# Kernel tuning notes

Measured on AMD Instinct MI355X. Metric: run time of the kernel, lower is better.

## Reference

```python
import jax, jax.numpy as jnp
import numpy as np

N_NODES = 100000
N_EDGES = 1600000
IN_CH = 128
OUT_CH = 32
HID = 2 * OUT_CH


def setup_inputs() -> dict:
    key = jax.random.key(0)
    k1, k2, k3, k4 = jax.random.split(key, 4)
    x = jax.random.normal(k1, (N_NODES, IN_CH), dtype=jnp.float32)
    edge_index = jax.random.randint(k2, (2, N_EDGES), 0, N_NODES, dtype=jnp.int64)
    W1 = jax.random.normal(k3, (IN_CH, HID), dtype=jnp.float32) / np.sqrt(IN_CH)
    b1 = jnp.zeros((HID,), dtype=jnp.float32)
    W2 = jax.random.normal(k4, (HID, OUT_CH), dtype=jnp.float32) / np.sqrt(HID)
    b2 = jnp.zeros((OUT_CH,), dtype=jnp.float32)
    return {"x": x, "edge_index": edge_index, "W1": W1, "b1": b1, "W2": W2, "b2": b2}


def _gcn_norm(edge_index, n_nodes):
    # GCNConv default: add self-loops, symmetric deg^{-1/2} normalization.
    loop = jnp.arange(n_nodes, dtype=edge_index.dtype)
    src = jnp.concatenate([edge_index[0], loop])
    dst = jnp.concatenate([edge_index[1], loop])
    deg = jax.ops.segment_sum(jnp.ones_like(dst, dtype=jnp.float32), dst, num_segments=n_nodes)
    dinv = jnp.where(deg > 0, jax.lax.rsqrt(deg), 0.0)
    norm = dinv[src] * dinv[dst]  # [E + N]
    return src, dst, norm


def _gcn_conv(h, W, b, src, dst, norm, n_nodes):
    m = h @ W                      # transform first (small GEMM)
    msg = m[src] * norm[:, None]   # gather + scale per edge
    agg = jax.ops.segment_sum(msg, dst, num_segments=n_nodes)  # scatter-add
    return agg + b


def reference(x, edge_index, W1, b1, W2, b2):
    n = x.shape[0]
    src, dst, norm = _gcn_norm(edge_index, n)
    h = jax.nn.relu(_gcn_conv(x, W1, b1, src, dst, norm, n))
    return _gcn_conv(h, W2, b2, src, dst, norm, n)
```

## Files before the change

kernel.cpp:

```cpp
#include <hip/hip_runtime.h>

#define IN_CH 128
#define HID 64
#define OUT_CH 32
#define BUCKET_CAP 6144
#define NB_MAX 512

typedef _Float16 f16x8 __attribute__((ext_vector_type(8)));
typedef float f32x4 __attribute__((ext_vector_type(4)));

__device__ __forceinline__ unsigned short f32_to_bf16(float f) {
    union { float f; unsigned int u; } v; v.f = f;
    unsigned int u = v.u;
    u += 0x7FFFu + ((u >> 16) & 1u);
    return (unsigned short)(u >> 16);
}
__device__ __forceinline__ float bf16_to_f32(unsigned short h) {
    union { unsigned int u; float f; } v; v.u = ((unsigned int)h) << 16;
    return v.f;
}
__device__ __forceinline__ float bf16_lo(unsigned int u) {
    union { unsigned int u; float f; } v; v.u = u << 16; return v.f;
}
__device__ __forceinline__ float bf16_hi(unsigned int u) {
    union { unsigned int u; float f; } v; v.u = u & 0xFFFF0000u; return v.f;
}

__device__ __forceinline__ int load_idx(const void* e, long long i, int is64) {
    if (is64) return ((const int*)e)[2 * i];
    return ((const int*)e)[i];
}

__global__ __launch_bounds__(256) void binA_kernel(
    const void* __restrict__ edges, long long E,
    int* __restrict__ bucket_cur, unsigned int* __restrict__ entries, int nb) {
    __shared__ int hist[NB_MAX];
    __shared__ int cbase[NB_MAX];
    __shared__ int s_is64;
    const int tid = threadIdx.x;

    if (tid < 64) {
        int v = ((const int*)edges)[2 * tid + 1];
        unsigned long long nz = __ballot(v != 0);
        if (tid == 0) s_is64 = (nz == 0ull) ? 1 : 0;
    }
    for (int i = tid; i < nb; i += 256) hist[i] = 0;
    __syncthreads();
    const int is64 = s_is64;

    const long long per = (E + gridDim.x - 1) / gridDim.x;
    const long long lo = blockIdx.x * per;
    const long long hi = (lo + per < E) ? lo + per : E;

    for (long long i = lo + tid; i < hi; i += 256) {
        int dst = load_idx(edges, E + i, is64);
        atomicAdd(&hist[dst >> 8], 1);
    }
    __syncthreads();
    for (int i = tid; i < nb; i += 256) {
        int c = hist[i];
        int base = (c > 0) ? atomicAdd(&bucket_cur[i], c) : 0;
        cbase[i] = base;
        hist[i] = 0;
    }
    __syncthreads();
    for (long long i = lo + tid; i < hi; i += 256) {
        int src = load_idx(edges, i, is64);
        int dst = load_idx(edges, E + i, is64);
        int b = dst >> 8;
        int rel = cbase[b] + atomicAdd(&hist[b], 1);
        if (rel < BUCKET_CAP)
            entries[(long long)b * BUCKET_CAP + rel] = ((unsigned)src << 8) | (unsigned)(dst & 255);
    }
}

__global__ __launch_bounds__(256) void binB1_kernel(
    const unsigned int* __restrict__ entries, const int* __restrict__ bucket_cur,
    int* __restrict__ counts, int* __restrict__ row_off, float* __restrict__ dinv,
    int n) {
    __shared__ int hist[256];
    __shared__ int scan[256];
    const int b   = blockIdx.x;
    const int tid = threadIdx.x;
    const long long seg = (long long)b * BUCKET_CAP;
    int cnt = bucket_cur[b];
    if (cnt > BUCKET_CAP) cnt = BUCKET_CAP;

    hist[tid] = 0;
    __syncthreads();
    for (int i = tid; i < cnt; i += 256)
        atomicAdd(&hist[entries[seg + i] & 255], 1);
    __syncthreads();

    int v = hist[tid];
    scan[tid] = v;
    __syncthreads();
    for (int off = 1; off < 256; off <<= 1) {
        int t = (tid >= off) ? scan[tid - off] : 0;
        __syncthreads();
        scan[tid] += t;
        __syncthreads();
    }
    int ex = scan[tid] - v;
    int node = (b << 8) + tid;
    if (node < n) {
        counts[node]  = v;
        row_off[node] = (int)seg + ex;
        dinv[node]    = rsqrtf((float)v + 1.0f);
    }
}

__global__ __launch_bounds__(256) void binB2_kernel(
    const unsigned int* __restrict__ entries, const int* __restrict__ bucket_cur,
    const int* __restrict__ row_off, const float* __restrict__ dinv,
    int2* __restrict__ ew, int n) {
    __shared__ int cur[256];
    __shared__ float ldi[256];
    const int b   = blockIdx.x;
    const int tid = threadIdx.x;
    const long long seg = (long long)b * BUCKET_CAP;
    int cnt = bucket_cur[b];
    if (cnt > BUCKET_CAP) cnt = BUCKET_CAP;

    int node = (b << 8) + tid;
    cur[tid] = (node < n) ? row_off[node] - (int)seg : 0;
    ldi[tid] = (node < n) ? dinv[node] : 0.f;
    __syncthreads();

    for (int i = tid; i < cnt; i += 256) {
        unsigned e = entries[seg + i];
        int d = (int)(e & 255u);
        int s = (int)(e >> 8);
        int r = atomicAdd(&cur[d], 1);
        float w = dinv[s] * ldi[d];
        int2 o; o.x = s; o.y = __float_as_int(w);
        ew[seg + r] = o;
    }
}

__global__ __launch_bounds__(256) void gemm1_kernel(
    const float* __restrict__ x, const float* __restrict__ W1,
    unsigned short* __restrict__ m1bf, int n) {
    const int lane = threadIdx.x & 63;
    const int wid  = threadIdx.x >> 6;
    const int m    = lane & 15;
    const int g    = lane >> 4;
    const int Rw   = blockIdx.x * 64 + wid * 16;

    f16x8 wf[4][4];
#pragma unroll
    for (int t = 0; t < 4; ++t) {
        const float* wp = W1 + (t * 32 + g * 8) * HID + m;
#pragma unroll
        for (int c = 0; c < 4; ++c) {
#pragma unroll
            for (int j = 0; j < 8; ++j)
                wf[c][t][j] = (_Float16)wp[j * HID + c * 16];
        }
    }

    int rl = Rw + m;
    if (rl >= n) rl = n - 1;
    const float* xr = x + (long long)rl * IN_CH;

    f32x4 acc[4] = {};

#pragma unroll
    for (int t = 0; t < 4; ++t) {
        float4 xa = *(const float4*)(xr + t * 32 + g * 8);
        float4 xb = *(const float4*)(xr + t * 32 + g * 8 + 4);
        f16x8 af;
        af[0] = (_Float16)xa.x; af[1] = (_Float16)xa.y;
        af[2] = (_Float16)xa.z; af[3] = (_Float16)xa.w;
        af[4] = (_Float16)xb.x; af[5] = (_Float16)xb.y;
        af[6] = (_Float16)xb.z; af[7] = (_Float16)xb.w;
#pragma unroll
        for (int c = 0; c < 4; ++c)
            acc[c] = __builtin_amdgcn_mfma_f32_16x16x32_f16(af, wf[c][t], acc[c], 0, 0, 0);
    }

#pragma unroll
    for (int c = 0; c < 4; ++c) {
#pragma unroll
        for (int r = 0; r < 4; ++r) {
            int row = Rw + g * 4 + r;
            if (row < n)
                m1bf[(long long)row * HID + c * 16 + m] = f32_to_bf16(acc[c][r]);
        }
    }
}

#define PADH 132
__global__ __launch_bounds__(256) void gemm2_kernel(
    const unsigned short* __restrict__ hbf, const float* __restrict__ W2,
    unsigned short* __restrict__ m2bf, int n) {
    __shared__ __align__(16) float sW[HID * OUT_CH];
    __shared__ __align__(16) float sH[HID * PADH];
    const int tid = threadIdx.x;

    {
        const float4* Wv = (const float4*)W2;
        float4* sWv = (float4*)sW;
        for (int i = tid; i < HID * OUT_CH / 4; i += 256) sWv[i] = Wv[i];
    }

    const int R0 = blockIdx.x * 128;
    for (int i = tid; i < 128 * 8; i += 256) {
        int r = i >> 3;
        int q = i & 7;
        int row = R0 + r;
        uint4 v = make_uint4(0u, 0u, 0u, 0u);
        if (row < n)
            v = ((const uint4*)(hbf + (long long)row * HID))[q];
        int k0 = q * 8;
        sH[(k0 + 0) * PADH + r] = bf16_lo(v.x);
        sH[(k0 + 1) * PADH + r] = bf16_hi(v.x);
        sH[(k0 + 2) * PADH + r] = bf16_lo(v.y);
        sH[(k0 + 3) * PADH + r] = bf16_hi(v.y);
        sH[(k0 + 4) * PADH + r] = bf16_lo(v.z);
        sH[(k0 + 5) * PADH + r] = bf16_hi(v.z);
        sH[(k0 + 6) * PADH + r] = bf16_lo(v.w);
        sH[(k0 + 7) * PADH + r] = bf16_hi(v.w);
    }
    __syncthreads();

    const int tx = tid & 7;
    const int ty = tid >> 3;
    float acc[4][4] = {};
    const float* pH = sH + ty * 4;
    const float* pW = sW + tx * 4;
#pragma unroll 8
    for (int k = 0; k < HID; ++k) {
        float4 hv = *(const float4*)(pH + k * PADH);
        float4 wv = *(const float4*)(pW + k * OUT_CH);
        acc[0][0] += hv.x * wv.x; acc[0][1] += hv.x * wv.y;
        acc[0][2] += hv.x * wv.z; acc[0][3] += hv.x * wv.w;
        acc[1][0] += hv.y * wv.x; acc[1][1] += hv.y * wv.y;
        acc[1][2] += hv.y * wv.z; acc[1][3] += hv.y * wv.w;
        acc[2][0] += hv.z * wv.x; acc[2][1] += hv.z * wv.y;
        acc[2][2] += hv.z * wv.z; acc[2][3] += hv.z * wv.w;
        acc[3][0] += hv.w * wv.x; acc[3][1] += hv.w * wv.y;
        acc[3][2] += hv.w * wv.z; acc[3][3] += hv.w * wv.w;
    }

#pragma unroll
    for (int i = 0; i < 4; ++i) {
        int row = R0 + ty * 4 + i;
        if (row < n) {
            ushort4 o;
            o.x = f32_to_bf16(acc[i][0]);
            o.y = f32_to_bf16(acc[i][1]);
            o.z = f32_to_bf16(acc[i][2]);
            o.w = f32_to_bf16(acc[i][3]);
            *(ushort4*)(m2bf + (long long)row * OUT_CH + tx * 4) = o;
        }
    }
}

__global__ __launch_bounds__(256) void gather64_kernel(
    const int* __restrict__ row_off, const int* __restrict__ counts,
    const int2* __restrict__ ew, const float* __restrict__ dinv,
    const unsigned short* __restrict__ m1bf, const float* __restrict__ b1,
    unsigned short* __restrict__ hbf, int n) {
    int node = blockIdx.x * 4 + (threadIdx.x >> 6);
    int lane = threadIdx.x & 63;
    if (node >= n) return;
    int start = __builtin_amdgcn_readfirstlane(row_off[node]);
    int cnt   = __builtin_amdgcn_readfirstlane(counts[node]);
    float dd  = dinv[node];
    float acc = bf16_to_f32(m1bf[(unsigned)(node * HID) + lane]) * dd * dd + b1[lane];
    int j = 0;
    for (; j + 15 < cnt; j += 16) {
        int2 e[16];
#pragma unroll
        for (int u = 0; u < 16; ++u) e[u] = ew[start + j + u];
        float v[16];
#pragma unroll
        for (int u = 0; u < 16; ++u)
            v[u] = bf16_to_f32(m1bf[(unsigned)(e[u].x * HID) + lane]);
#pragma unroll
        for (int u = 0; u < 16; ++u) acc += v[u] * __int_as_float(e[u].y);
    }
    for (; j + 7 < cnt; j += 8) {
        int2 e[8];
#pragma unroll
        for (int u = 0; u < 8; ++u) e[u] = ew[start + j + u];
        float v[8];
#pragma unroll
        for (int u = 0; u < 8; ++u)
            v[u] = bf16_to_f32(m1bf[(unsigned)(e[u].x * HID) + lane]);
#pragma unroll
        for (int u = 0; u < 8; ++u) acc += v[u] * __int_as_float(e[u].y);
    }
    for (; j + 3 < cnt; j += 4) {
        int2 e[4];
#pragma unroll
        for (int u = 0; u < 4; ++u) e[u] = ew[start + j + u];
        float v[4];
#pragma unroll
        for (int u = 0; u < 4; ++u)
            v[u] = bf16_to_f32(m1bf[(unsigned)(e[u].x * HID) + lane]);
#pragma unroll
        for (int u = 0; u < 4; ++u) acc += v[u] * __int_as_float(e[u].y);
    }
    for (; j < cnt; ++j) {
        int2 e = ew[start + j];
        acc += bf16_to_f32(m1bf[(unsigned)(e.x * HID) + lane]) * __int_as_float(e.y);
    }
    hbf[(unsigned)(node * HID) + lane] = f32_to_bf16(fmaxf(acc, 0.f));
}

__global__ __launch_bounds__(256) void gather32_kernel(
    const int* __restrict__ row_off, const int* __restrict__ counts,
    const int2* __restrict__ ew, const float* __restrict__ dinv,
    const unsigned short* __restrict__ m2bf, const float* __restrict__ b2,
    float* __restrict__ out, int n) {
    int node = blockIdx.x * 4 + (threadIdx.x >> 6);
    int lane = threadIdx.x & 63;
    int c    = lane & 31;
    int p    = lane >> 5;
    if (node >= n) return;
    int start = __builtin_amdgcn_readfirstlane(row_off[node]);
    int cnt   = __builtin_amdgcn_readfirstlane(counts[node]);
    float dd  = dinv[node];
    float acc = 0.f;
    int j = 0;
    for (; j + 15 < cnt; j += 16) {
        int2 e[16];
#pragma unroll
        for (int u = 0; u < 16; ++u) e[u] = ew[start + j + u];
#pragma unroll
        for (int u = 0; u < 8; ++u) {
            int2 ea = e[2 * u];
            int2 eb = e[2 * u + 1];
            int   sx = p ? eb.x : ea.x;
            float wv = __int_as_float(p ? eb.y : ea.y);
            acc += bf16_to_f32(m2bf[(unsigned)(sx * OUT_CH) + c]) * wv;
        }
    }
    for (; j + 7 < cnt; j += 8) {
        int2 e[8];
#pragma unroll
        for (int u = 0; u < 8; ++u) e[u] = ew[start + j + u];
#pragma unroll
        for (int u = 0; u < 4; ++u) {
            int2 ea = e[2 * u];
            int2 eb = e[2 * u + 1];
            int   sx = p ? eb.x : ea.x;
            float wv = __int_as_float(p ? eb.y : ea.y);
            acc += bf16_to_f32(m2bf[(unsigned)(sx * OUT_CH) + c]) * wv;
        }
    }
    for (; j + 3 < cnt; j += 4) {
        int2 e[4];
#pragma unroll
        for (int u = 0; u < 4; ++u) e[u] = ew[start + j + u];
#pragma unroll
        for (int u = 0; u < 2; ++u) {
            int2 ea = e[2 * u];
            int2 eb = e[2 * u + 1];
            int   sx = p ? eb.x : ea.x;
            float wv = __int_as_float(p ? eb.y : ea.y);
            acc += bf16_to_f32(m2bf[(unsigned)(sx * OUT_CH) + c]) * wv;
        }
    }
    for (; j < cnt; j += 2) {
        int q = j + p;
        int2 e = ew[start + ((q < cnt) ? q : j)];
        float w = (q < cnt) ? __int_as_float(e.y) : 0.f;
        acc += bf16_to_f32(m2bf[(unsigned)(e.x * OUT_CH) + c]) * w;
    }
    acc += __shfl_xor(acc, 32, 64);
    if (p == 0) {
        float self = bf16_to_f32(m2bf[(unsigned)(node * OUT_CH) + c]);
        out[(unsigned)(node * OUT_CH) + c] = acc + self * dd * dd + b2[c];
    }
}

extern "C" void kernel_launch(void* const* d_in, const int* in_sizes, int n_in,
                              void* d_out, int out_size, void* d_ws, size_t ws_size,
                              hipStream_t stream) {
    const float* x     = (const float*)d_in[0];
    const void*  edges = d_in[1];
    const float* W1    = (const float*)d_in[2];
    const float* b1    = (const float*)d_in[3];
    const float* W2    = (const float*)d_in[4];
    const float* b2    = (const float*)d_in[5];
    float* out = (float*)d_out;

    const int n = in_sizes[0] / IN_CH;
    const long long E = (long long)in_sizes[1] / 2;
    const int nb = (n + 255) / 256;

    float* ws         = (float*)d_ws;
    float* dinv       = ws;
    unsigned short* m1bf = (unsigned short*)(ws + n);
    unsigned short* m2bf = m1bf;
    float* agg        = ws + n + (long long)n * HID / 2;
    unsigned int* entries = (unsigned int*)agg;
    unsigned short* hbf   = (unsigned short*)agg;
    int*   counts     = (int*)(agg + (long long)n * HID);
    int*   row_off    = counts + n;
    int*   bucket_cur = row_off + n;
    int2*  ew         = (int2*)(bucket_cur + NB_MAX);

    hipMemsetAsync(bucket_cur, 0, NB_MAX * sizeof(int), stream);

    binA_kernel<<<256, 256, 0, stream>>>(edges, E, bucket_cur, entries, nb);
    binB1_kernel<<<nb, 256, 0, stream>>>(entries, bucket_cur, counts, row_off, dinv, n);
    binB2_kernel<<<nb, 256, 0, stream>>>(entries, bucket_cur, row_off, dinv, ew, n);

    gemm1_kernel<<<(n + 63) / 64, 256, 0, stream>>>(x, W1, m1bf, n);
    gather64_kernel<<<(n + 3) / 4, 256, 0, stream>>>(
        row_off, counts, ew, dinv, m1bf, b1, hbf, n);

    gemm2_kernel<<<(n + 127) / 128, 256, 0, stream>>>(hbf, W2, m2bf, n);
    gather32_kernel<<<(n + 3) / 4, 256, 0, stream>>>(
        row_off, counts, ew, dinv, m2bf, b2, out, n);
}
```

Measured before the change: 257.9 us.

## Gather multiple edges per wavefront with 8-byte vector loads in both aggregation kernels

Both gather kernels now split each wavefront into edge groups: each lane loads four bf16 features at once as a uint2, and several edges are processed in parallel across lane groups. Partial sums are combined with cross-lane xor shuffles, and a few lanes write the final row as a vector store. The goal is fewer, wider memory requests per edge and more edge-level parallelism in flight. In exchange it adds shuffle reductions, leaves most lanes idle during the epilogue, and uses a shallower unroll than the previous 16-edge batching.

Measured after the change: 266.5 us. 3.3% more time.

```diff
diff --git a/kernel.cpp b/kernel.cpp
--- a/kernel.cpp
+++ b/kernel.cpp
@@ -267,47 +267,50 @@
     if (node >= n) return;
     int start = __builtin_amdgcn_readfirstlane(row_off[node]);
     int cnt   = __builtin_amdgcn_readfirstlane(counts[node]);
-    float dd  = dinv[node];
-    float acc = bf16_to_f32(m1bf[(unsigned)(node * HID) + lane]) * dd * dd + b1[lane];
+    const int eg = lane >> 4;
+    const int q  = lane & 15;
+
+    float a0 = 0.f, a1 = 0.f, a2 = 0.f, a3 = 0.f;
     int j = 0;
-    for (; j + 15 < cnt; j += 16) {
-        int2 e[16];
-#pragma unroll
-        for (int u = 0; u < 16; ++u) e[u] = ew[start + j + u];
-        float v[16];
-#pragma unroll
-        for (int u = 0; u < 16; ++u)
-            v[u] = bf16_to_f32(m1bf[(unsigned)(e[u].x * HID) + lane]);
-#pragma unroll
-        for (int u = 0; u < 16; ++u) acc += v[u] * __int_as_float(e[u].y);
-    }
     for (; j + 7 < cnt; j += 8) {
-        int2 e[8];
-#pragma unroll
-        for (int u = 0; u < 8; ++u) e[u] = ew[start + j + u];
-        float v[8];
-#pragma unroll
-        for (int u = 0; u < 8; ++u)
-            v[u] = bf16_to_f32(m1bf[(unsigned)(e[u].x * HID) + lane]);
-#pragma unroll
-        for (int u = 0; u < 8; ++u) acc += v[u] * __int_as_float(e[u].y);
-    }
-    for (; j + 3 < cnt; j += 4) {
-        int2 e[4];
-#pragma unroll
-        for (int u = 0; u < 4; ++u) e[u] = ew[start + j + u];
-        float v[4];
-#pragma unroll
-        for (int u = 0; u < 4; ++u)
-            v[u] = bf16_to_f32(m1bf[(unsigned)(e[u].x * HID) + lane]);
-#pragma unroll
-        for (int u = 0; u < 4; ++u) acc += v[u] * __int_as_float(e[u].y);
-    }
-    for (; j < cnt; ++j) {
-        int2 e = ew[start + j];
-        acc += bf16_to_f32(m1bf[(unsigned)(e.x * HID) + lane]) * __int_as_float(e.y);
-    }
-    hbf[(unsigned)(node * HID) + lane] = f32_to_bf16(fmaxf(acc, 0.f));
+        int2 ea = ew[start + j + eg];
+        int2 eb = ew[start + j + 4 + eg];
+        uint2 va = *(const uint2*)(m1bf + (unsigned)(ea.x * HID) + q * 4);
+        uint2 vb = *(const uint2*)(m1bf + (unsigned)(eb.x * HID) + q * 4);
+        float wa = __int_as_float(ea.y);
+        float wb = __int_as_float(eb.y);
+        a0 += bf16_lo(va.x) * wa; a1 += bf16_hi(va.x) * wa;
+        a2 += bf16_lo(va.y) * wa; a3 += bf16_hi(va.y) * wa;
+        a0 += bf16_lo(vb.x) * wb; a1 += bf16_hi(vb.x) * wb;
+        a2 += bf16_lo(vb.y) * wb; a3 += bf16_hi(vb.y) * wb;
+    }
+    for (; j < cnt; j += 4) {
+        int idx  = j + eg;
+        int cidx = (idx < cnt) ? idx : cnt - 1;
+        int2 e = ew[start + cidx];
+        float w = (idx < cnt) ? __int_as_float(e.y) : 0.f;
+        uint2 v = *(const uint2*)(m1bf + (unsigned)(e.x * HID) + q * 4);
+        a0 += bf16_lo(v.x) * w; a1 += bf16_hi(v.x) * w;
+        a2 += bf16_lo(v.y) * w; a3 += bf16_hi(v.y) * w;
+    }
+
+    a0 += __shfl_xor(a0, 16, 64); a1 += __shfl_xor(a1, 16, 64);
+    a2 += __shfl_xor(a2, 16, 64); a3 += __shfl_xor(a3, 16, 64);
+    a0 += __shfl_xor(a0, 32, 64); a1 += __shfl_xor(a1, 32, 64);
+    a2 += __shfl_xor(a2, 32, 64); a3 += __shfl_xor(a3, 32, 64);
+
+    if (lane < 16) {
+        float dd = dinv[node];
+        float ss = dd * dd;
+        uint2 sv = *(const uint2*)(m1bf + (unsigned)(node * HID) + lane * 4);
+        float4 bv = *(const float4*)(b1 + lane * 4);
+        ushort4 o;
+        o.x = f32_to_bf16(fmaxf(a0 + bf16_lo(sv.x) * ss + bv.x, 0.f));
+        o.y = f32_to_bf16(fmaxf(a1 + bf16_hi(sv.x) * ss + bv.y, 0.f));
+        o.z = f32_to_bf16(fmaxf(a2 + bf16_lo(sv.y) * ss + bv.z, 0.f));
+        o.w = f32_to_bf16(fmaxf(a3 + bf16_hi(sv.y) * ss + bv.w, 0.f));
+        *(ushort4*)(hbf + (unsigned)(node * HID) + lane * 4) = o;
+    }
 }
 
 __global__ __launch_bounds__(256) void gather32_kernel(
@@ -317,63 +320,54 @@
     float* __restrict__ out, int n) {
     int node = blockIdx.x * 4 + (threadIdx.x >> 6);
     int lane = threadIdx.x & 63;
-    int c    = lane & 31;
-    int p    = lane >> 5;
     if (node >= n) return;
     int start = __builtin_amdgcn_readfirstlane(row_off[node]);
     int cnt   = __builtin_amdgcn_readfirstlane(counts[node]);
-    float dd  = dinv[node];
-    float acc = 0.f;
+    const int eg = lane >> 3;
+    const int q  = lane & 7;
+
+    float a0 = 0.f, a1 = 0.f, a2 = 0.f, a3 = 0.f;
     int j = 0;
     for (; j + 15 < cnt; j += 16) {
-        int2 e[16];
-#pragma unroll
-        for (int u = 0; u < 16; ++u) e[u] = ew[start + j + u];
-#pragma unroll
-        for (int u = 0; u < 8; ++u) {
-            int2 ea = e[2 * u];
-            int2 eb = e[2 * u + 1];
-            int   sx = p ? eb.x : ea.x;
-            float wv = __int_as_float(p ? eb.y : ea.y);
-            acc += bf16_to_f32(m2bf[(unsigned)(sx * OUT_CH) + c]) * wv;
-        }
-    }
-    for (; j + 7 < cnt; j += 8) {
-        int2 e[8];
-#pragma unroll
-        for (int u = 0; u < 8; ++u) e[u] = ew[start + j + u];
-#pragma unroll
-        for (int u = 0; u < 4; ++u) {
-            int2 ea = e[2 * u];
-            int2 eb = e[2 * u + 1];
-            int   sx = p ? eb.x : ea.x;
-            float wv = __int_as_float(p ? eb.y : ea.y);
-            acc += bf16_to_f32(m2bf[(unsigned)(sx * OUT_CH) + c]) * wv;
-        }
-    }
-    for (; j + 3 < cnt; j += 4) {
-        int2 e[4];
-#pragma unroll
-        for (int u = 0; u < 4; ++u) e[u] = ew[start + j + u];
-#pragma unroll
-        for (int u = 0; u < 2; ++u) {
-            int2 ea = e[2 * u];
-            int2 eb = e[2 * u + 1];
-            int   sx = p ? eb.x : ea.x;
-            float wv = __int_as_float(p ? eb.y : ea.y);
-            acc += bf16_to_f32(m2bf[(unsigned)(sx * OUT_CH) + c]) * wv;
-        }
-    }
-    for (; j < cnt; j += 2) {
-        int q = j + p;
-        int2 e = ew[start + ((q < cnt) ? q : j)];
-        float w = (q < cnt) ? __int_as_float(e.y) : 0.f;
-        acc += bf16_to_f32(m2bf[(unsigned)(e.x * OUT_CH) + c]) * w;
-    }
-    acc += __shfl_xor(acc, 32, 64);
-    if (p == 0) {
-        float self = bf16_to_f32(m2bf[(unsigned)(node * OUT_CH) + c]);
-        out[(unsigned)(node * OUT_CH) + c] = acc + self * dd * dd + b2[c];
+        int2 ea = ew[start + j + eg];
+        int2 eb = ew[start + j + 8 + eg];
+        uint2 va = *(const uint2*)(m2bf + (unsigned)(ea.x * OUT_CH) + q * 4);
+        uint2 vb = *(const uint2*)(m2bf + (unsigned)(eb.x * OUT_CH) + q * 4);
+        float wa = __int_as_float(ea.y);
+        float wb = __int_as_float(eb.y);
+        a0 += bf16_lo(va.x) * wa; a1 += bf16_hi(va.x) * wa;
+        a2 += bf16_lo(va.y) * wa; a3 += bf16_hi(va.y) * wa;
+        a0 += bf16_lo(vb.x) * wb; a1 += bf16_hi(vb.x) * wb;
+        a2 += bf16_lo(vb.y) * wb; a3 += bf16_hi(vb.y) * wb;
+    }
+    for (; j < cnt; j += 8) {
+        int idx  = j + eg;
+        int cidx = (idx < cnt) ? idx : cnt - 1;
+        int2 e = ew[start + cidx];
+        float w = (idx < cnt) ? __int_as_float(e.y) : 0.f;
+        uint2 v = *(const uint2*)(m2bf + (unsigned)(e.x * OUT_CH) + q * 4);
+        a0 += bf16_lo(v.x) * w; a1 += bf16_hi(v.x) * w;
+        a2 += bf16_lo(v.y) * w; a3 += bf16_hi(v.y) * w;
+    }
+
+    a0 += __shfl_xor(a0,  8, 64); a1 += __shfl_xor(a1,  8, 64);
+    a2 += __shfl_xor(a2,  8, 64); a3 += __shfl_xor(a3,  8, 64);
+    a0 += __shfl_xor(a0, 16, 64); a1 += __shfl_xor(a1, 16, 64);
+    a2 += __shfl_xor(a2, 16, 64); a3 += __shfl_xor(a3, 16, 64);
+    a0 += __shfl_xor(a0, 32, 64); a1 += __shfl_xor(a1, 32, 64);
+    a2 += __shfl_xor(a2, 32, 64); a3 += __shfl_xor(a3, 32, 64);
+
+    if (lane < 8) {
+        float dd = dinv[node];
+        float ss = dd * dd;
+        uint2 sv = *(const uint2*)(m2bf + (unsigned)(node * OUT_CH) + lane * 4);
+        float4 bv = *(const float4*)(b2 + lane * 4);
+        float4 o;
+        o.x = a0 + bf16_lo(sv.x) * ss + bv.x;
+        o.y = a1 + bf16_hi(sv.x) * ss + bv.y;
+        o.z = a2 + bf16_lo(sv.y) * ss + bv.z;
+        o.w = a3 + bf16_hi(sv.y) * ss + bv.w;
+        *(float4*)(out + (unsigned)(node * OUT_CH) + lane * 4) = o;
     }
 }
 
```

## Map two nodes per wavefront in both GCN gather kernels

Applied to the files above, without the earlier changes.

Both gather kernels now assign one node per 32 lanes instead of one per 64-lane wavefront, so each wave processes two nodes. The 64-channel layer loads two bf16 values per lane as a 32-bit word and keeps two accumulators. The 32-channel layer drops the split-edge parity trick and its cross-half shuffle reduction. The aim is to halve the wave count per node and widen per-lane loads. The cost is that the two half-waves can now have different edge counts, so loops diverge, and the scalar readfirstlane edge-loop bounds become per-lane vector values.

Result: no change. 257.5 us (-0.2%).

```diff
diff --git a/kernel.cpp b/kernel.cpp
--- a/kernel.cpp
+++ b/kernel.cpp
@@ -262,52 +262,74 @@
     const int2* __restrict__ ew, const float* __restrict__ dinv,
     const unsigned short* __restrict__ m1bf, const float* __restrict__ b1,
     unsigned short* __restrict__ hbf, int n) {
-    int node = blockIdx.x * 4 + (threadIdx.x >> 6);
-    int lane = threadIdx.x & 63;
+    const int node = blockIdx.x * 8 + (threadIdx.x >> 5);
+    const int l    = threadIdx.x & 31;
     if (node >= n) return;
-    int start = __builtin_amdgcn_readfirstlane(row_off[node]);
-    int cnt   = __builtin_amdgcn_readfirstlane(counts[node]);
-    float dd  = dinv[node];
-    float acc = bf16_to_f32(m1bf[(unsigned)(node * HID) + lane]) * dd * dd + b1[lane];
+    const int start = row_off[node];
+    const int cnt   = counts[node];
+
+    float a0 = 0.f, a1 = 0.f;
     int j = 0;
     for (; j + 15 < cnt; j += 16) {
         int2 e[16];
 #pragma unroll
         for (int u = 0; u < 16; ++u) e[u] = ew[start + j + u];
-        float v[16];
+        unsigned v[16];
 #pragma unroll
         for (int u = 0; u < 16; ++u)
-            v[u] = bf16_to_f32(m1bf[(unsigned)(e[u].x * HID) + lane]);
-#pragma unroll
-        for (int u = 0; u < 16; ++u) acc += v[u] * __int_as_float(e[u].y);
+            v[u] = *(const unsigned*)(m1bf + (unsigned)(e[u].x * HID) + l * 2);
+#pragma unroll
+        for (int u = 0; u < 16; ++u) {
+            float w = __int_as_float(e[u].y);
+            a0 += bf16_lo(v[u]) * w;
+            a1 += bf16_hi(v[u]) * w;
+        }
     }
     for (; j + 7 < cnt; j += 8) {
         int2 e[8];
 #pragma unroll
         for (int u = 0; u < 8; ++u) e[u] = ew[start + j + u];
-        float v[8];
+        unsigned v[8];
 #pragma unroll
         for (int u = 0; u < 8; ++u)
-            v[u] = bf16_to_f32(m1bf[(unsigned)(e[u].x * HID) + lane]);
-#pragma unroll
-        for (int u = 0; u < 8; ++u) acc += v[u] * __int_as_float(e[u].y);
+            v[u] = *(const unsigned*)(m1bf + (unsigned)(e[u].x * HID) + l * 2);
+#pragma unroll
+        for (int u = 0; u < 8; ++u) {
+            float w = __int_as_float(e[u].y);
+            a0 += bf16_lo(v[u]) * w;
+            a1 += bf16_hi(v[u]) * w;
+        }
     }
     for (; j + 3 < cnt; j += 4) {
         int2 e[4];
 #pragma unroll
         for (int u = 0; u < 4; ++u) e[u] = ew[start + j + u];
-        float v[4];
+        unsigned v[4];
 #pragma unroll
         for (int u = 0; u < 4; ++u)
-            v[u] = bf16_to_f32(m1bf[(unsigned)(e[u].x * HID) + lane]);
-#pragma unroll
-        for (int u = 0; u < 4; ++u) acc += v[u] * __int_as_float(e[u].y);
+            v[u] = *(const unsigned*)(m1bf + (unsigned)(e[u].x * HID) + l * 2);
+#pragma unroll
+        for (int u = 0; u < 4; ++u) {
+            float w = __int_as_float(e[u].y);
+            a0 += bf16_lo(v[u]) * w;
+            a1 += bf16_hi(v[u]) * w;
+        }
     }
     for (; j < cnt; ++j) {
         int2 e = ew[start + j];
-        acc += bf16_to_f32(m1bf[(unsigned)(e.x * HID) + lane]) * __int_as_float(e.y);
-    }
-    hbf[(unsigned)(node * HID) + lane] = f32_to_bf16(fmaxf(acc, 0.f));
+        unsigned v = *(const unsigned*)(m1bf + (unsigned)(e.x * HID) + l * 2);
+        float w = __int_as_float(e.y);
+        a0 += bf16_lo(v) * w;
+        a1 += bf16_hi(v) * w;
+    }
+
+    float dd = dinv[node];
+    float ss = dd * dd;
+    unsigned sv = *(const unsigned*)(m1bf + (unsigned)(node * HID) + l * 2);
+    ushort2 o;
+    o.x = f32_to_bf16(fmaxf(a0 + bf16_lo(sv) * ss + b1[l * 2],     0.f));
+    o.y = f32_to_bf16(fmaxf(a1 + bf16_hi(sv) * ss + b1[l * 2 + 1], 0.f));
+    *(ushort2*)(hbf + (unsigned)(node * HID) + l * 2) = o;
 }
 
 __global__ __launch_bounds__(256) void gather32_kernel(
@@ -315,66 +337,58 @@
     const int2* __restrict__ ew, const float* __restrict__ dinv,
     const unsigned short* __restrict__ m2bf, const float* __restrict__ b2,
     float* __restrict__ out, int n) {
-    int node = blockIdx.x * 4 + (threadIdx.x >> 6);
-    int lane = threadIdx.x & 63;
-    int c    = lane & 31;
-    int p    = lane >> 5;
+    const int node = blockIdx.x * 8 + (threadIdx.x >> 5);
+    const int l    = threadIdx.x & 31;
     if (node >= n) return;
-    int start = __builtin_amdgcn_readfirstlane(row_off[node]);
-    int cnt   = __builtin_amdgcn_readfirstlane(counts[node]);
-    float dd  = dinv[node];
+    const int start = row_off[node];
+    const int cnt   = counts[node];
+
     float acc = 0.f;
     int j = 0;
     for (; j + 15 < cnt; j += 16) {
         int2 e[16];
 #pragma unroll
         for (int u = 0; u < 16; ++u) e[u] = ew[start + j + u];
-#pragma unroll
-        for (int u = 0; u < 8; ++u) {
-            int2 ea = e[2 * u];
-            int2 eb = e[2 * u + 1];
-            int   sx = p ? eb.x : ea.x;
-            float wv = __int_as_float(p ? eb.y : ea.y);
-            acc += bf16_to_f32(m2bf[(unsigned)(sx * OUT_CH) + c]) * wv;
-        }
+        unsigned short v[16];
+#pragma unroll
+        for (int u = 0; u < 16; ++u)
+            v[u] = m2bf[(unsigned)(e[u].x * OUT_CH) + l];
+#pragma unroll
+        for (int u = 0; u < 16; ++u)
+            acc += bf16_to_f32(v[u]) * __int_as_float(e[u].y);
     }
     for (; j + 7 < cnt; j += 8) {
         int2 e[8];
 #pragma unroll
         for (int u = 0; u < 8; ++u) e[u] = ew[start + j + u];
-#pragma unroll
-        for (int u = 0; u < 4; ++u) {
-            int2 ea = e[2 * u];
-            int2 eb = e[2 * u + 1];
-            int   sx = p ? eb.x : ea.x;
-            float wv = __int_as_float(p ? eb.y : ea.y);
-            acc += bf16_to_f32(m2bf[(unsigned)(sx * OUT_CH) + c]) * wv;
-        }
+        unsigned short v[8];
+#pragma unroll
+        for (int u = 0; u < 8; ++u)
+            v[u] = m2bf[(unsigned)(e[u].x * OUT_CH) + l];
+#pragma unroll
+        for (int u = 0; u < 8; ++u)
+            acc += bf16_to_f32(v[u]) * __int_as_float(e[u].y);
     }
     for (; j + 3 < cnt; j += 4) {
         int2 e[4];
 #pragma unroll
         for (int u = 0; u < 4; ++u) e[u] = ew[start + j + u];
-#pragma unroll
-        for (int u = 0; u < 2; ++u) {
-            int2 ea = e[2 * u];
-            int2 eb = e[2 * u + 1];
-            int   sx = p ? eb.x : ea.x;
-            float wv = __int_as_float(p ? eb.y : ea.y);
-            acc += bf16_to_f32(m2bf[(unsigned)(sx * OUT_CH) + c]) * wv;
-        }
-    }
-    for (; j < cnt; j += 2) {
-        int q = j + p;
-        int2 e = ew[start + ((q < cnt) ? q : j)];
-        float w = (q < cnt) ? __int_as_float(e.y) : 0.f;
-        acc += bf16_to_f32(m2bf[(unsigned)(e.x * OUT_CH) + c]) * w;
-    }
-    acc += __shfl_xor(acc, 32, 64);
-    if (p == 0) {
-        float self = bf16_to_f32(m2bf[(unsigned)(node * OUT_CH) + c]);
-        out[(unsigned)(node * OUT_CH) + c] = acc + self * dd * dd + b2[c];
-    }
+        unsigned short v[4];
+#pragma unroll
+        for (int u = 0; u < 4; ++u)
+            v[u] = m2bf[(unsigned)(e[u].x * OUT_CH) + l];
+#pragma unroll
+        for (int u = 0; u < 4; ++u)
+            acc += bf16_to_f32(v[u]) * __int_as_float(e[u].y);
+    }
+    for (; j < cnt; ++j) {
+        int2 e = ew[start + j];
+        acc += bf16_to_f32(m2bf[(unsigned)(e.x * OUT_CH) + l]) * __int_as_float(e.y);
+    }
+
+    float dd = dinv[node];
+    float self = bf16_to_f32(m2bf[(unsigned)(node * OUT_CH) + l]);
+    out[(unsigned)(node * OUT_CH) + l] = acc + self * dd * dd + b2[l];
 }
 
 extern "C" void kernel_launch(void* const* d_in, const int* in_sizes, int n_in,
@@ -411,10 +425,10 @@
     binB2_kernel<<<nb, 256, 0, stream>>>(entries, bucket_cur, row_off, dinv, ew, n);
 
     gemm1_kernel<<<(n + 63) / 64, 256, 0, stream>>>(x, W1, m1bf, n);
-    gather64_kernel<<<(n + 3) / 4, 256, 0, stream>>>(
+    gather64_kernel<<<(n + 7) / 8, 256, 0, stream>>>(
         row_off, counts, ew, dinv, m1bf, b1, hbf, n);
 
     gemm2_kernel<<<(n + 127) / 128, 256, 0, stream>>>(hbf, W2, m2bf, n);
-    gather32_kernel<<<(n + 3) / 4, 256, 0, stream>>>(
+    gather32_kernel<<<(n + 7) / 8, 256, 0, stream>>>(
         row_off, counts, ew, dinv, m2bf, b2, out, n);
 }
```
